# Kernel tuning notes

Measured on AMD Instinct MI355X. Metric: run time of the kernel, lower is better.

The kernel has to match this reference:

```python
import jax, jax.numpy as jnp
import numpy as np
import math

FEATURE_DIM = 64; HIDDEN = 128; NUM_BLOCKS = 4; NUM_ITERS = 4
R = 3; KSIZE = 5; BANDS = 16; TEMP = 0.1
WW = 2 * R + 1; P = WW * WW                      # 7x7 = 49 correlation window
POS_DIM = 3 * (2 * BANDS + 1)                    # 99
IN_DIM = P + POS_DIM + HIDDEN                    # 276
B, Q, T, HF, WF = 1, 256, 64, 128, 128


def setup_inputs() -> dict:
    key = jax.random.key(0)
    ks = jax.random.split(key, 10)
    stride = 4
    extent = jnp.array([WF * stride - 1.0, HF * stride - 1.0], jnp.float32)
    return {
        "query_features": jax.random.normal(ks[0], (B, Q, FEATURE_DIM), jnp.float32),
        "feature_maps": jax.random.normal(ks[1], (B, T, FEATURE_DIM, HF, WF), jnp.float32),
        "positions": jax.random.uniform(ks[2], (B, Q, T, 2), jnp.float32) * extent,
        "feature_stride": stride,
        "w_in": jax.random.normal(ks[3], (IN_DIM, HIDDEN), jnp.float32) * 0.02,
        "b_in": jnp.zeros((HIDDEN,), jnp.float32),
        "ln1_g": jnp.ones((NUM_BLOCKS, HIDDEN), jnp.float32),
        "ln1_b": jnp.zeros((NUM_BLOCKS, HIDDEN), jnp.float32),
        "conv_w": jax.random.normal(ks[4], (NUM_BLOCKS, HIDDEN, 1, KSIZE), jnp.float32) * 0.1,
        "conv_b": jnp.zeros((NUM_BLOCKS, HIDDEN), jnp.float32),
        "ln2_g": jnp.ones((NUM_BLOCKS, HIDDEN), jnp.float32),
        "ln2_b": jnp.zeros((NUM_BLOCKS, HIDDEN), jnp.float32),
        "mlp_w1": jax.random.normal(ks[5], (NUM_BLOCKS, HIDDEN, 2 * HIDDEN), jnp.float32) * 0.02,
        "mlp_b1": jnp.zeros((NUM_BLOCKS, 2 * HIDDEN), jnp.float32),
        "mlp_w2": jax.random.normal(ks[6], (NUM_BLOCKS, 2 * HIDDEN, HIDDEN), jnp.float32) * 0.02,
        "mlp_b2": jnp.zeros((NUM_BLOCKS, HIDDEN), jnp.float32),
        "w_delta": jnp.zeros((HIDDEN, 2), jnp.float32),   # delta head zero-init per _init_weights
        "b_delta": jnp.zeros((2,), jnp.float32),
        "vis_w1": jax.random.normal(ks[7], (HIDDEN, HIDDEN // 2), jnp.float32) * 0.02,
        "vis_b1": jnp.zeros((HIDDEN // 2,), jnp.float32),
        "vis_w2": jax.random.normal(ks[8], (HIDDEN // 2, 1), jnp.float32) * 0.02,
        "vis_b2": jnp.zeros((1,), jnp.float32),
    }


def _layer_norm(x, g, b):
    m = jnp.mean(x, -1, keepdims=True)
    v = jnp.mean((x - m) ** 2, -1, keepdims=True)
    return (x - m) * jax.lax.rsqrt(v + 1e-5) * g + b


def _fourier(coords):
    # sin/cos Fourier encoding + raw coords: [..., D] -> [..., D*(2*BANDS+1)]
    freqs = (2.0 ** jnp.linspace(0.0, math.log2(512.0), BANDS)) * jnp.pi
    x = coords[..., None] * freqs                       # [..., D, BANDS]
    enc = jnp.concatenate([jnp.sin(x), jnp.cos(x)], -1) # [..., D, 2*BANDS]
    enc = enc.reshape(enc.shape[:-2] + (-1,))
    return jnp.concatenate([coords, enc], -1)


def _bilinear(fm, xy):
    # fm: [N, H, W, C] (channels-last); xy: [N, M, 2] feature-grid coords (x, y).
    # Border-clamped bilinear interpolation.
    H, W = fm.shape[1], fm.shape[2]
    x, y = xy[..., 0], xy[..., 1]
    x0f, y0f = jnp.floor(x), jnp.floor(y)
    wx, wy = (x - x0f)[..., None], (y - y0f)[..., None]
    x0 = jnp.clip(x0f.astype(jnp.int32), 0, W - 1)
    x1 = jnp.clip(x0f.astype(jnp.int32) + 1, 0, W - 1)
    y0 = jnp.clip(y0f.astype(jnp.int32), 0, H - 1)
    y1 = jnp.clip(y0f.astype(jnp.int32) + 1, 0, H - 1)
    b = jnp.arange(fm.shape[0])[:, None]
    v00 = fm[b, y0, x0]; v01 = fm[b, y0, x1]
    v10 = fm[b, y1, x0]; v11 = fm[b, y1, x1]
    return (v00 * (1 - wx) + v01 * wx) * (1 - wy) + (v10 * (1 - wx) + v11 * wx) * wy


def _extract_local_correlation(qf, fmaps, pos, stride):
    # qf: [B,Q,C], fmaps: [B,T,C,H,W], pos: [B,Q,T,2] pixel coords.
    Bb, Tt, C, Hf, Wf = fmaps.shape
    Qq = qf.shape[1]
    offs = jnp.arange(-R, R + 1, dtype=pos.dtype)
    oy, ox = jnp.meshgrid(offs, offs, indexing='ij')
    grid = jnp.stack([ox.reshape(-1), oy.reshape(-1)], -1)        # [P,2], x fastest
    off_pix = grid * float(stride)                                 # pixel-unit offsets
    # sampling coords in feature-grid units: pos/stride + offset cells
    sc = pos[:, :, :, None, :] / float(stride) + grid              # [B,Q,T,P,2]
    sc = jnp.transpose(sc, (0, 2, 1, 3, 4)).reshape(Bb * Tt, Qq * P, 2)
    fm = jnp.transpose(fmaps.reshape(Bb * Tt, C, Hf, Wf), (0, 2, 3, 1))
    sampled = _bilinear(fm, sc).reshape(Bb, Tt, Qq, P, C)
    corr = jnp.einsum('btqpc,bqc->bqtp', sampled, qf)              # [B,Q,T,P]
    probs = jax.nn.softmax(corr * (1.0 / max(TEMP, 1e-6)), axis=-1)
    sa_delta = jnp.einsum('bqtp,pd->bqtd', probs, off_pix)         # [B,Q,T,2]
    return corr, sa_delta


def reference(query_features, feature_maps, positions, feature_stride,
              w_in, b_in, ln1_g, ln1_b, conv_w, conv_b, ln2_g, ln2_b,
              mlp_w1, mlp_b1, mlp_w2, mlp_b2, w_delta, b_delta,
              vis_w1, vis_b1, vis_w2, vis_b2):
    Bb, Qq, Tt, _ = positions.shape
    coords = positions
    hidden = jnp.zeros((Bb, Qq, Tt, HIDDEN), positions.dtype)
    t_idx = jnp.linspace(0.0, 1.0, Tt, dtype=positions.dtype).reshape(1, 1, Tt, 1)
    norm_xy = jnp.array([feature_maps.shape[4] * feature_stride,
                         feature_maps.shape[3] * feature_stride], positions.dtype)
    for _ in range(NUM_ITERS):   # weight-shared refinement iterations
        corr, sa = _extract_local_correlation(query_features, feature_maps, coords, feature_stride)
        coords = coords + sa
        pos_in = jnp.concatenate(
            [coords / norm_xy, jnp.broadcast_to(t_idx, (Bb, Qq, Tt, 1))], -1)  # [B,Q,T,3]
        pe = _fourier(pos_in)                                                   # [B,Q,T,99]
        h = jnp.concatenate([corr, pe, hidden], -1) @ w_in + b_in              # [B,Q,T,D]
        h = h.reshape(Bb * Qq, Tt, HIDDEN)
        for i in range(NUM_BLOCKS):
            z = _layer_norm(h, ln1_g[i], ln1_b[i])
            z = jnp.transpose(z, (0, 2, 1))                                     # [BQ,D,T]
            z = jax.lax.conv_general_dilated(
                z, conv_w[i], (1,), [(KSIZE // 2, KSIZE // 2)],
                feature_group_count=HIDDEN, dimension_numbers=('NCH', 'OIH', 'NCH'))
            z = z + conv_b[i][None, :, None]
            h = h + jnp.transpose(z, (0, 2, 1))
            z = _layer_norm(h, ln2_g[i], ln2_b[i])
            h = h + (jax.nn.gelu(z @ mlp_w1[i] + mlp_b1[i], approximate=False)
                     @ mlp_w2[i] + mlp_b2[i])
        h = h.reshape(Bb, Qq, Tt, HIDDEN)
        hidden = h
        coords = coords + h @ w_delta + b_delta
    vis = (jax.nn.gelu(hidden @ vis_w1 + vis_b1, approximate=False) @ vis_w2 + vis_b2)
    return coords, vis
```

## Files before the change

kernel.cpp:

```cpp
#include <hip/hip_runtime.h>
#include <hip/hip_bf16.h>
#include <math.h>

#define PN 49

typedef short v8s __attribute__((ext_vector_type(8)));
typedef float v4f __attribute__((ext_vector_type(4)));
typedef unsigned short us8 __attribute__((ext_vector_type(8)));

#define MFMA_BF16(a,b,c) __builtin_amdgcn_mfma_f32_16x16x32_bf16(a,b,c,0,0,0)

__device__ __forceinline__ unsigned short f2bf(float x) {
    union { float f; unsigned u; } v; v.f = x;
    return (unsigned short)((v.u + 0x7FFFu + ((v.u >> 16) & 1u)) >> 16);
}
__device__ __forceinline__ float bf2f(unsigned short h) {
    union { unsigned u; float f; } v; v.u = ((unsigned)h) << 16;
    return v.f;
}
__device__ __forceinline__ int BIDX(int r, int c) {
    return r * 128 + ((((c >> 3) ^ (r & 15)) << 3) | (c & 7));
}
__device__ __forceinline__ float gelu_exact(float x) {
    return 0.5f * x * (1.0f + erff(x * 0.70710678118654752f));
}
__device__ __forceinline__ float pe_enc(int jj, float px, float py, float ti) {
    const int d = jj >> 5, rr = jj & 31, bnd = rr & 15, isc = rr >> 4;
    const float bv = (d == 0) ? px : ((d == 1) ? py : ti);
    const float a = bv * (exp2f(0.6f * (float)bnd) * 3.14159265358979f);
    return isc ? __cosf(a) : __sinf(a);
}

__global__ __launch_bounds__(256) void repack_kernel(
    const float* __restrict__ w_in, const float* __restrict__ w1,
    const float* __restrict__ w2, unsigned short* __restrict__ pk)
{
    const int id = blockIdx.x * 256 + threadIdx.x;
    if (id >= 584 * 64) return;
    const int chunk = id >> 6, lane = id & 63;
    const int quad = lane >> 4, l15 = lane & 15;
    float v[8];
    if (chunk < 72) {
        const int ks = chunk >> 3, nt = chunk & 7, n = nt * 16 + l15;
#pragma unroll
        for (int j = 0; j < 8; ++j) {
            int src;
            if (ks < 4) src = ks * 32 + quad * 8 + j;
            else if (ks == 4) { const int kl = quad * 8 + j; src = (kl < 20) ? 128 + kl : -1; }
            else src = 148 + (ks - 5) * 32 + quad * 8 + j;
            v[j] = (src >= 0) ? w_in[src * 128 + n] : 0.f;
        }
    } else if (chunk < 328) {
        const int c = chunk - 72, blk = c >> 6, r = c & 63, ks = r >> 4, nt = r & 15;
#pragma unroll
        for (int j = 0; j < 8; ++j)
            v[j] = w1[blk * 32768 + (ks * 32 + quad * 8 + j) * 256 + nt * 16 + l15];
    } else {
        const int c = chunk - 328, blk = c >> 6, r = c & 63, ks = r >> 3, nt = r & 7;
#pragma unroll
        for (int j = 0; j < 8; ++j)
            v[j] = w2[blk * 32768 + (ks * 32 + quad * 8 + j) * 128 + nt * 16 + l15];
    }
    unsigned short* dst = &pk[(size_t)id * 8];
#pragma unroll
    for (int j = 0; j < 8; ++j) dst[j] = f2bf(v[j]);
}

__global__ __launch_bounds__(256) void corr_kernel(
    const float* __restrict__ qf, const float* __restrict__ fm,
    float* __restrict__ coords, float* __restrict__ corr_ws,
    const int* __restrict__ stride_p)
{
    __shared__ float sQ[4][64];
    __shared__ float sD[4][64];
    const int wv   = threadIdx.x >> 6;
    const int lane = threadIdx.x & 63;
    const int t    = blockIdx.x >> 6;
    const int q    = ((blockIdx.x & 63) << 2) + wv;

    sQ[wv][lane] = qf[(q << 6) + lane];

    const int   st     = stride_p[0];
    const float inv_st = 1.0f / (float)st;
    const int   rowg   = (q << 6) + t;
    const float cx = coords[rowg * 2 + 0];
    const float cy = coords[rowg * 2 + 1];
    const float xc = cx * inv_st, yc = cy * inv_st;
    const float x0f = floorf(xc), y0f = floorf(yc);
    const float fx = xc - x0f, fy = yc - y0f;
    const int ix0 = (int)x0f - 3, iy0 = (int)y0f - 3;
    const int gx = min(max(ix0 + (lane & 7), 0), 127);
    const int gy = min(max(iy0 + (lane >> 3), 0), 127);
    const float* base = fm + ((size_t)t << 20) + (gy << 7) + gx;

    __syncthreads();
    float dot = 0.0f;
#pragma unroll 32
    for (int c = 0; c < 64; ++c) dot += base[(size_t)c << 14] * sQ[wv][c];
    sD[wv][lane] = dot;
    __syncthreads();

    const int p = lane;
    float corrv = 0.0f;
    float mval  = -INFINITY;
    int gxc = 0, gyc = 0;
    if (p < PN) {
        gyc = p / 7; gxc = p - gyc * 7;
        const float c00 = sD[wv][gyc * 8 + gxc],     c01 = sD[wv][gyc * 8 + gxc + 1];
        const float c10 = sD[wv][gyc * 8 + gxc + 8], c11 = sD[wv][gyc * 8 + gxc + 9];
        corrv = (1.0f - fy) * ((1.0f - fx) * c00 + fx * c01)
              +          fy * ((1.0f - fx) * c10 + fx * c11);
        corr_ws[(size_t)rowg * PN + p] = corrv;
        mval = corrv * 10.0f;
    }
    float mm = mval;
#pragma unroll
    for (int off = 32; off; off >>= 1) mm = fmaxf(mm, __shfl_xor(mm, off));
    float ex = 0.0f, sax = 0.0f, say = 0.0f;
    if (p < PN) {
        ex  = expf(mval - mm);
        sax = ex * (float)((gxc - 3) * st);
        say = ex * (float)((gyc - 3) * st);
    }
#pragma unroll
    for (int off = 32; off; off >>= 1) {
        ex  += __shfl_xor(ex,  off);
        sax += __shfl_xor(sax, off);
        say += __shfl_xor(say, off);
    }
    if (lane == 0) {
        coords[rowg * 2 + 0] = cx + sax / ex;
        coords[rowg * 2 + 1] = cy + say / ex;
    }
}

__global__ __launch_bounds__(512, 4) void mega_kernel(
    const float* __restrict__ corr_ws, float* __restrict__ coords,
    float* __restrict__ H, const unsigned short* __restrict__ wpk,
    const float* __restrict__ b_in,
    const float* __restrict__ ln1_g, const float* __restrict__ ln1_b,
    const float* __restrict__ conv_w, const float* __restrict__ conv_b,
    const float* __restrict__ ln2_g, const float* __restrict__ ln2_b,
    const float* __restrict__ b1, const float* __restrict__ b2,
    const float* __restrict__ w_delta, const float* __restrict__ b_delta,
    const int* __restrict__ stride_p)
{
    __shared__ float          zs[64 * 128];
    __shared__ unsigned short hbf[64 * 128];
    __shared__ unsigned short sbf[64 * 128];

    const unsigned short* wpk_in = wpk;
    const unsigned short* wpk1   = wpk + 72 * 512;
    const unsigned short* wpk2   = wpk + 328 * 512;

    const int q    = blockIdx.x;
    const int tid  = threadIdx.x;
    const int lane = tid & 63;
    const int wid  = __builtin_amdgcn_readfirstlane(tid >> 6);
    const int l15  = lane & 15, quad = lane >> 4;
    const int mt   = wid & 3, ntg = wid >> 2;
    const float inv_norm = 1.0f / (128.0f * (float)stride_p[0]);

    for (int i = tid; i < 2048; i += 512) {
        const float4 v = ((const float4*)&H[(size_t)q * 8192])[i];
        const int r = i >> 5, c = (i & 31) << 2;
        unsigned short* d = &hbf[BIDX(r, c)];
        d[0] = f2bf(v.x); d[1] = f2bf(v.y); d[2] = f2bf(v.z); d[3] = f2bf(v.w);
    }
    for (int idx = tid; idx < 64 * 128; idx += 512) {
        const int r = idx >> 7, c = idx & 127;
        float v;
        if (c < 49) v = corr_ws[((size_t)((q << 6) + r)) * PN + c];
        else {
            const int j = c - 49;
            const float px = coords[(((q << 6) + r) << 1) + 0] * inv_norm;
            const float py = coords[(((q << 6) + r) << 1) + 1] * inv_norm;
            const float ti = (float)r * (1.0f / 63.0f);
            v = (j == 0) ? px : (j == 1) ? py : (j == 2) ? ti : pe_enc(j - 3, px, py, ti);
        }
        sbf[BIDX(r, c)] = f2bf(v);
    }
    __syncthreads();

    {
        v4f acc[4];
#pragma unroll
        for (int i = 0; i < 4; ++i) acc[i] = v4f{0.f, 0.f, 0.f, 0.f};
        const int arow = mt * 16 + l15;
#pragma unroll
        for (int ks = 0; ks < 4; ++ks) {
            const v8s a = *(const v8s*)&sbf[arow * 128 + (((ks * 4 + quad) ^ (arow & 15)) << 3)];
#pragma unroll
            for (int i = 0; i < 4; ++i) {
                const v8s b = *(const v8s*)&wpk_in[(size_t)((ks * 8 + ntg * 4 + i) * 64 + lane) * 8];
                acc[i] = MFMA_BF16(a, b, acc[i]);
            }
        }
#pragma unroll
        for (int ks = 5; ks < 9; ++ks) {
            const v8s a = *(const v8s*)&hbf[arow * 128 + ((((ks - 5) * 4 + quad) ^ (arow & 15)) << 3)];
#pragma unroll
            for (int i = 0; i < 4; ++i) {
                const v8s b = *(const v8s*)&wpk_in[(size_t)((ks * 8 + ntg * 4 + i) * 64 + lane) * 8];
                acc[i] = MFMA_BF16(a, b, acc[i]);
            }
        }
        __syncthreads();
        for (int idx = tid; idx < 64 * 32; idx += 512) {
            const int r = idx >> 5, c2 = idx & 31;
            float v = 0.f;
            if (c2 < 20) {
                const float px = coords[(((q << 6) + r) << 1) + 0] * inv_norm;
                const float py = coords[(((q << 6) + r) << 1) + 1] * inv_norm;
                const float ti = (float)r * (1.0f / 63.0f);
                v = pe_enc(76 + c2, px, py, ti);
            }
            sbf[BIDX(r, c2)] = f2bf(v);
        }
        __syncthreads();
        {
            const v8s a = *(const v8s*)&sbf[arow * 128 + ((quad ^ (arow & 15)) << 3)];
#pragma unroll
            for (int i = 0; i < 4; ++i) {
                const v8s b = *(const v8s*)&wpk_in[(size_t)((4 * 8 + ntg * 4 + i) * 64 + lane) * 8];
                acc[i] = MFMA_BF16(a, b, acc[i]);
            }
        }
        const int rowb = mt * 16 + quad * 4;
#pragma unroll
        for (int i = 0; i < 4; ++i) {
            const int col = (ntg * 4 + i) * 16 + l15;
            const float bi = b_in[col];
#pragma unroll
            for (int g = 0; g < 4; ++g) zs[(rowb + g) * 128 + col] = acc[i][g] + bi;
        }
    }
    __syncthreads();

    for (int blk = 0; blk < 4; ++blk) {
        {
            const int row = tid >> 3, part = tid & 7;
            float v[16];
#pragma unroll
            for (int x = 0; x < 4; ++x)
                *(float4*)&v[4 * x] = *(const float4*)&zs[row * 128 + part * 16 + 4 * x];
            float s1 = 0.f, s2 = 0.f;
#pragma unroll
            for (int j = 0; j < 16; ++j) { s1 += v[j]; s2 += v[j] * v[j]; }
            s1 += __shfl_xor(s1, 1); s1 += __shfl_xor(s1, 2); s1 += __shfl_xor(s1, 4);
            s2 += __shfl_xor(s2, 1); s2 += __shfl_xor(s2, 2); s2 += __shfl_xor(s2, 4);
            const float m  = s1 * 0.0078125f;
            const float rs = rsqrtf(fmaxf(s2 * 0.0078125f - m * m, 0.f) + 1e-5f);
            unsigned short o[16];
#pragma unroll
            for (int j = 0; j < 16; ++j)
                o[j] = f2bf((v[j] - m) * rs * ln1_g[blk * 128 + part * 16 + j] + ln1_b[blk * 128 + part * 16 + j]);
#pragma unroll
            for (int x = 0; x < 2; ++x)
                *(us8*)&hbf[row * 128 + (((part * 2 + x) ^ (row & 15)) << 3)] = *(us8*)&o[8 * x];
        }
        __syncthreads();
        {
            const int c = tid & 127, tg = tid >> 7;
            float cw[5];
#pragma unroll
            for (int k = 0; k < 5; ++k) cw[k] = conv_w[(blk * 128 + c) * 5 + k];
            const float cb = conv_b[blk * 128 + c];
            float ring[20];
#pragma unroll
            for (int i = 0; i < 20; ++i) {
                const int tt = tg * 16 - 2 + i;
                ring[i] = (tt >= 0 && tt < 64) ? bf2f(hbf[BIDX(tt, c)]) : 0.f;
            }
#pragma unroll
            for (int s = 0; s < 16; ++s) {
                float o = cb;
#pragma unroll
                for (int k = 0; k < 5; ++k) o += ring[s + k] * cw[k];
                zs[(tg * 16 + s) * 128 + c] += o;
            }
        }
        __syncthreads();
        {
            const int row = tid >> 3, part = tid & 7;
            float v[16];
#pragma unroll
            for (int x = 0; x < 4; ++x)
                *(float4*)&v[4 * x] = *(const float4*)&zs[row * 128 + part * 16 + 4 * x];
            float s1 = 0.f, s2 = 0.f;
#pragma unroll
            for (int j = 0; j < 16; ++j) { s1 += v[j]; s2 += v[j] * v[j]; }
            s1 += __shfl_xor(s1, 1); s1 += __shfl_xor(s1, 2); s1 += __shfl_xor(s1, 4);
            s2 += __shfl_xor(s2, 1); s2 += __shfl_xor(s2, 2); s2 += __shfl_xor(s2, 4);
            const float m  = s1 * 0.0078125f;
            const float rs = rsqrtf(fmaxf(s2 * 0.0078125f - m * m, 0.f) + 1e-5f);
            unsigned short o[16];
#pragma unroll
            for (int j = 0; j < 16; ++j)
                o[j] = f2bf((v[j] - m) * rs * ln2_g[blk * 128 + part * 16 + j] + ln2_b[blk * 128 + part * 16 + j]);
#pragma unroll
            for (int x = 0; x < 2; ++x)
                *(us8*)&hbf[row * 128 + (((part * 2 + x) ^ (row & 15)) << 3)] = *(us8*)&o[8 * x];
        }
        __syncthreads();
        v4f u[8];
        const int arow = mt * 16 + l15;
        {
            v8s afr[4];
#pragma unroll
            for (int ks = 0; ks < 4; ++ks)
                afr[ks] = *(const v8s*)&hbf[arow * 128 + (((ks * 4 + quad) ^ (arow & 15)) << 3)];
#pragma unroll
            for (int i = 0; i < 8; ++i) u[i] = v4f{0.f, 0.f, 0.f, 0.f};
#pragma unroll
            for (int ks = 0; ks < 4; ++ks)
#pragma unroll
                for (int i = 0; i < 8; ++i) {
                    const int nt = i * 2 + ntg;
                    const v8s b = *(const v8s*)&wpk1[(size_t)(((blk * 4 + ks) * 16 + nt) * 64 + lane) * 8];
                    u[i] = MFMA_BF16(afr[ks], b, u[i]);
                }
#pragma unroll
            for (int i = 0; i < 8; ++i) {
                const float b1v = b1[blk * 256 + (i * 2 + ntg) * 16 + l15];
#pragma unroll
                for (int g = 0; g < 4; ++g) u[i][g] = gelu_exact(u[i][g] + b1v);
            }
        }
        const int rowb = mt * 16 + quad * 4;
#pragma unroll
        for (int i = 0; i < 4; ++i) {
            const int ucol = (i * 2 + ntg) * 16 + l15;
#pragma unroll
            for (int g = 0; g < 4; ++g) sbf[BIDX(rowb + g, ucol)] = f2bf(u[i][g]);
        }
        __syncthreads();
        v4f c2[4];
#pragma unroll
        for (int i = 0; i < 4; ++i) c2[i] = v4f{0.f, 0.f, 0.f, 0.f};
#pragma unroll
        for (int ks = 0; ks < 4; ++ks) {
            const v8s a = *(const v8s*)&sbf[arow * 128 + (((ks * 4 + quad) ^ (arow & 15)) << 3)];
#pragma unroll
            for (int i = 0; i < 4; ++i) {
                const v8s b = *(const v8s*)&wpk2[(size_t)(((blk * 8 + ks) * 8 + ntg * 4 + i) * 64 + lane) * 8];
                c2[i] = MFMA_BF16(a, b, c2[i]);
            }
        }
        __syncthreads();
#pragma unroll
        for (int i = 4; i < 8; ++i) {
            const int ucol = (i * 2 + ntg) * 16 + l15 - 128;
#pragma unroll
            for (int g = 0; g < 4; ++g) sbf[BIDX(rowb + g, ucol)] = f2bf(u[i][g]);
        }
        __syncthreads();
#pragma unroll
        for (int ks = 0; ks < 4; ++ks) {
            const v8s a = *(const v8s*)&sbf[arow * 128 + (((ks * 4 + quad) ^ (arow & 15)) << 3)];
#pragma unroll
            for (int i = 0; i < 4; ++i) {
                const v8s b = *(const v8s*)&wpk2[(size_t)(((blk * 8 + 4 + ks) * 8 + ntg * 4 + i) * 64 + lane) * 8];
                c2[i] = MFMA_BF16(a, b, c2[i]);
            }
        }
#pragma unroll
        for (int i = 0; i < 4; ++i) {
            const int col = (ntg * 4 + i) * 16 + l15;
            const float b2v = b2[blk * 128 + col];
#pragma unroll
            for (int g = 0; g < 4; ++g) zs[(rowb + g) * 128 + col] += c2[i][g] + b2v;
        }
        __syncthreads();
    }

    {
        const int row = tid >> 3, part = tid & 7;
        float dx = 0.f, dy = 0.f;
#pragma unroll
        for (int j = 0; j < 16; ++j) {
            const int c = part * 16 + j;
            const float hv = zs[row * 128 + c];
            dx += hv * w_delta[2 * c];
            dy += hv * w_delta[2 * c + 1];
        }
        dx += __shfl_xor(dx, 1); dx += __shfl_xor(dx, 2); dx += __shfl_xor(dx, 4);
        dy += __shfl_xor(dy, 1); dy += __shfl_xor(dy, 2); dy += __shfl_xor(dy, 4);
        if (part == 0) {
            coords[(((q << 6) + row) << 1) + 0] += dx + b_delta[0];
            coords[(((q << 6) + row) << 1) + 1] += dy + b_delta[1];
        }
    }
    for (int i = tid; i < 2048; i += 512)
        ((float4*)&H[(size_t)q * 8192])[i] = ((const float4*)zs)[i];
}

__global__ __launch_bounds__(256) void vis_kernel(
    const float* __restrict__ H,
    const float* __restrict__ vw1, const float* __restrict__ vb1,
    const float* __restrict__ vw2, const float* __restrict__ vb2,
    float* __restrict__ out)
{
    const int row = (blockIdx.x << 2) + (threadIdx.x >> 6);
    const int j   = threadIdx.x & 63;
    float acc = vb1[j];
    const float* hr = &H[(size_t)row << 7];
#pragma unroll 16
    for (int k = 0; k < 128; ++k) acc += hr[k] * vw1[(k << 6) + j];
    float pv = gelu_exact(acc) * vw2[j];
#pragma unroll
    for (int off = 32; off; off >>= 1) pv += __shfl_xor(pv, off);
    if (j == 0) out[row] = pv + vb2[0];
}

extern "C" void kernel_launch(void* const* d_in, const int* in_sizes, int n_in,
                              void* d_out, int out_size, void* d_ws, size_t ws_size,
                              hipStream_t stream) {
    const float* qf       = (const float*)d_in[0];
    const float* fm       = (const float*)d_in[1];
    const float* pos      = (const float*)d_in[2];
    const int*   stride_p = (const int*)  d_in[3];
    const float* w_in     = (const float*)d_in[4];
    const float* b_in     = (const float*)d_in[5];
    const float* ln1_g    = (const float*)d_in[6];
    const float* ln1_b    = (const float*)d_in[7];
    const float* conv_w   = (const float*)d_in[8];
    const float* conv_b   = (const float*)d_in[9];
    const float* ln2_g    = (const float*)d_in[10];
    const float* ln2_b    = (const float*)d_in[11];
    const float* mlp_w1   = (const float*)d_in[12];
    const float* mlp_b1   = (const float*)d_in[13];
    const float* mlp_w2   = (const float*)d_in[14];
    const float* mlp_b2   = (const float*)d_in[15];
    const float* w_delta  = (const float*)d_in[16];
    const float* b_delta  = (const float*)d_in[17];
    const float* vis_w1   = (const float*)d_in[18];
    const float* vis_b1   = (const float*)d_in[19];
    const float* vis_w2   = (const float*)d_in[20];
    const float* vis_b2   = (const float*)d_in[21];

    float* Wf      = (float*)d_ws;
    float* coords  = Wf;
    float* corr_ws = Wf + 32768;
    float* H       = Wf + 32768 + 802816;
    unsigned short* wpk = (unsigned short*)(Wf + 2932736);

    repack_kernel<<<dim3(146), dim3(256), 0, stream>>>(w_in, mlp_w1, mlp_w2, wpk);
    hipMemcpyAsync(coords, pos, 32768 * sizeof(float), hipMemcpyDeviceToDevice, stream);
    hipMemsetAsync(H, 0, 2097152 * sizeof(float), stream);

    for (int it = 0; it < 4; ++it) {
        corr_kernel<<<dim3(4096), dim3(256), 0, stream>>>(qf, fm, coords, corr_ws, stride_p);
        mega_kernel<<<dim3(256), dim3(512), 0, stream>>>(
            corr_ws, coords, H, wpk, b_in, ln1_g, ln1_b, conv_w, conv_b,
            ln2_g, ln2_b, mlp_b1, mlp_b2, w_delta, b_delta, stride_p);
    }
    vis_kernel<<<dim3(4096), dim3(256), 0, stream>>>(
        H, vis_w1, vis_b1, vis_w2, vis_b2, ((float*)d_out) + 32768);
    hipMemcpyAsync(d_out, coords, 32768 * sizeof(float), hipMemcpyDeviceToDevice, stream);
}
```

Baseline: 1.739 ms.

## Split mega kernel per query into two time halves with conv halo recompute

Each query's 64-step sequence is now handled by two blocks, each covering 32 output time steps plus an 8-step halo on each side (48 rows). The halo is recomputed so the stacked depthwise convolutions stay correct without inter-block communication. This doubles the grid to 512 blocks of 768 threads so more CUs are busy, and threads are remapped accordingly. The cost is about 50% redundant compute on the halo rows plus extra index and boundary checks.

```diff
diff --git a/kernel.cpp b/kernel.cpp
--- a/kernel.cpp
+++ b/kernel.cpp
@@ -3,6 +3,9 @@
 #include <math.h>
 
 #define PN 49
+#define RB 48
+#define OUT0 8
+#define OUTN 32
 
 typedef short v8s __attribute__((ext_vector_type(8)));
 typedef float v4f __attribute__((ext_vector_type(4)));
@@ -134,7 +137,7 @@
     }
 }
 
-__global__ __launch_bounds__(512, 4) void mega_kernel(
+__global__ __launch_bounds__(768, 6) void mega_kernel(
     const float* __restrict__ corr_ws, float* __restrict__ coords,
     float* __restrict__ H, const unsigned short* __restrict__ wpk,
     const float* __restrict__ b_in,
@@ -145,54 +148,68 @@
     const float* __restrict__ w_delta, const float* __restrict__ b_delta,
     const int* __restrict__ stride_p)
 {
-    __shared__ float          zs[64 * 128];
-    __shared__ unsigned short hbf[64 * 128];
-    __shared__ unsigned short sbf[64 * 128];
+    __shared__ float          zs[RB * 128];
+    __shared__ unsigned short hbf[RB * 128];
+    __shared__ unsigned short sbf[RB * 128];
+    __shared__ float          crd[RB][2];
 
     const unsigned short* wpk_in = wpk;
     const unsigned short* wpk1   = wpk + 72 * 512;
     const unsigned short* wpk2   = wpk + 328 * 512;
 
-    const int q    = blockIdx.x;
-    const int tid  = threadIdx.x;
-    const int lane = tid & 63;
-    const int wid  = __builtin_amdgcn_readfirstlane(tid >> 6);
-    const int l15  = lane & 15, quad = lane >> 4;
-    const int mt   = wid & 3, ntg = wid >> 2;
+    const int q     = blockIdx.x >> 1;
+    const int half  = blockIdx.x & 1;
+    const int baset = half * 32 - OUT0;
+    const int tid   = threadIdx.x;
+    const int lane  = tid & 63;
+    const int wid   = __builtin_amdgcn_readfirstlane(tid >> 6);
+    const int l15   = lane & 15, quad = lane >> 4;
+    const int mt    = wid >> 2, ntg = wid & 3;
     const float inv_norm = 1.0f / (128.0f * (float)stride_p[0]);
 
-    for (int i = tid; i < 2048; i += 512) {
-        const float4 v = ((const float4*)&H[(size_t)q * 8192])[i];
-        const int r = i >> 5, c = (i & 31) << 2;
-        unsigned short* d = &hbf[BIDX(r, c)];
+    if (tid < RB * 2) {
+        const int rr = tid >> 1, xy = tid & 1;
+        const int tc = min(max(baset + rr, 0), 63);
+        crd[rr][xy] = coords[(((q << 6) + tc) << 1) + xy];
+    }
+    for (int i = tid; i < RB * 32; i += 768) {
+        const int r = i >> 5, c0 = (i & 31) << 2;
+        const int t = baset + r;
+        float4 v = make_float4(0.f, 0.f, 0.f, 0.f);
+        if (t >= 0 && t < 64) v = *(const float4*)&H[(size_t)q * 8192 + t * 128 + c0];
+        unsigned short* d = &hbf[BIDX(r, c0)];
         d[0] = f2bf(v.x); d[1] = f2bf(v.y); d[2] = f2bf(v.z); d[3] = f2bf(v.w);
     }
-    for (int idx = tid; idx < 64 * 128; idx += 512) {
+    __syncthreads();
+    for (int idx = tid; idx < RB * 128; idx += 768) {
         const int r = idx >> 7, c = idx & 127;
+        const int t = baset + r;
         float v;
-        if (c < 49) v = corr_ws[((size_t)((q << 6) + r)) * PN + c];
+        if (c < 49) v = (t >= 0 && t < 64) ? corr_ws[((size_t)((q << 6) + t)) * PN + c] : 0.f;
         else {
             const int j = c - 49;
-            const float px = coords[(((q << 6) + r) << 1) + 0] * inv_norm;
-            const float py = coords[(((q << 6) + r) << 1) + 1] * inv_norm;
-            const float ti = (float)r * (1.0f / 63.0f);
+            const float px = crd[r][0] * inv_norm;
+            const float py = crd[r][1] * inv_norm;
+            const float ti = (float)min(max(t, 0), 63) * (1.0f / 63.0f);
             v = (j == 0) ? px : (j == 1) ? py : (j == 2) ? ti : pe_enc(j - 3, px, py, ti);
         }
         sbf[BIDX(r, c)] = f2bf(v);
     }
     __syncthreads();
 
+    const int arow = mt * 16 + l15;
+    const int rowb = mt * 16 + quad * 4;
+
     {
-        v4f acc[4];
-#pragma unroll
-        for (int i = 0; i < 4; ++i) acc[i] = v4f{0.f, 0.f, 0.f, 0.f};
-        const int arow = mt * 16 + l15;
+        v4f acc[2];
+#pragma unroll
+        for (int i = 0; i < 2; ++i) acc[i] = v4f{0.f, 0.f, 0.f, 0.f};
 #pragma unroll
         for (int ks = 0; ks < 4; ++ks) {
             const v8s a = *(const v8s*)&sbf[arow * 128 + (((ks * 4 + quad) ^ (arow & 15)) << 3)];
 #pragma unroll
-            for (int i = 0; i < 4; ++i) {
-                const v8s b = *(const v8s*)&wpk_in[(size_t)((ks * 8 + ntg * 4 + i) * 64 + lane) * 8];
+            for (int i = 0; i < 2; ++i) {
+                const v8s b = *(const v8s*)&wpk_in[(size_t)((ks * 8 + ntg * 2 + i) * 64 + lane) * 8];
                 acc[i] = MFMA_BF16(a, b, acc[i]);
             }
         }
@@ -200,19 +217,20 @@
         for (int ks = 5; ks < 9; ++ks) {
             const v8s a = *(const v8s*)&hbf[arow * 128 + ((((ks - 5) * 4 + quad) ^ (arow & 15)) << 3)];
 #pragma unroll
-            for (int i = 0; i < 4; ++i) {
-                const v8s b = *(const v8s*)&wpk_in[(size_t)((ks * 8 + ntg * 4 + i) * 64 + lane) * 8];
+            for (int i = 0; i < 2; ++i) {
+                const v8s b = *(const v8s*)&wpk_in[(size_t)((ks * 8 + ntg * 2 + i) * 64 + lane) * 8];
                 acc[i] = MFMA_BF16(a, b, acc[i]);
             }
         }
         __syncthreads();
-        for (int idx = tid; idx < 64 * 32; idx += 512) {
+        for (int idx = tid; idx < RB * 32; idx += 768) {
             const int r = idx >> 5, c2 = idx & 31;
             float v = 0.f;
             if (c2 < 20) {
-                const float px = coords[(((q << 6) + r) << 1) + 0] * inv_norm;
-                const float py = coords[(((q << 6) + r) << 1) + 1] * inv_norm;
-                const float ti = (float)r * (1.0f / 63.0f);
+                const int t = baset + r;
+                const float px = crd[r][0] * inv_norm;
+                const float py = crd[r][1] * inv_norm;
+                const float ti = (float)min(max(t, 0), 63) * (1.0f / 63.0f);
                 v = pe_enc(76 + c2, px, py, ti);
             }
             sbf[BIDX(r, c2)] = f2bf(v);
@@ -221,15 +239,14 @@
         {
             const v8s a = *(const v8s*)&sbf[arow * 128 + ((quad ^ (arow & 15)) << 3)];
 #pragma unroll
-            for (int i = 0; i < 4; ++i) {
-                const v8s b = *(const v8s*)&wpk_in[(size_t)((4 * 8 + ntg * 4 + i) * 64 + lane) * 8];
+            for (int i = 0; i < 2; ++i) {
+                const v8s b = *(const v8s*)&wpk_in[(size_t)((4 * 8 + ntg * 2 + i) * 64 + lane) * 8];
                 acc[i] = MFMA_BF16(a, b, acc[i]);
             }
         }
-        const int rowb = mt * 16 + quad * 4;
-#pragma unroll
-        for (int i = 0; i < 4; ++i) {
-            const int col = (ntg * 4 + i) * 16 + l15;
+#pragma unroll
+        for (int i = 0; i < 2; ++i) {
+            const int col = (ntg * 2 + i) * 16 + l15;
             const float bi = b_in[col];
 #pragma unroll
             for (int g = 0; g < 4; ++g) zs[(rowb + g) * 128 + col] = acc[i][g] + bi;
@@ -239,25 +256,24 @@
 
     for (int blk = 0; blk < 4; ++blk) {
         {
-            const int row = tid >> 3, part = tid & 7;
-            float v[16];
-#pragma unroll
-            for (int x = 0; x < 4; ++x)
-                *(float4*)&v[4 * x] = *(const float4*)&zs[row * 128 + part * 16 + 4 * x];
+            const int row = tid >> 4, part = tid & 15;
+            float v[8];
+            *(float4*)&v[0] = *(const float4*)&zs[row * 128 + part * 8];
+            *(float4*)&v[4] = *(const float4*)&zs[row * 128 + part * 8 + 4];
             float s1 = 0.f, s2 = 0.f;
 #pragma unroll
-            for (int j = 0; j < 16; ++j) { s1 += v[j]; s2 += v[j] * v[j]; }
-            s1 += __shfl_xor(s1, 1); s1 += __shfl_xor(s1, 2); s1 += __shfl_xor(s1, 4);
-            s2 += __shfl_xor(s2, 1); s2 += __shfl_xor(s2, 2); s2 += __shfl_xor(s2, 4);
+            for (int j = 0; j < 8; ++j) { s1 += v[j]; s2 += v[j] * v[j]; }
+            s1 += __shfl_xor(s1, 1); s1 += __shfl_xor(s1, 2);
+            s1 += __shfl_xor(s1, 4); s1 += __shfl_xor(s1, 8);
+            s2 += __shfl_xor(s2, 1); s2 += __shfl_xor(s2, 2);
+            s2 += __shfl_xor(s2, 4); s2 += __shfl_xor(s2, 8);
             const float m  = s1 * 0.0078125f;
             const float rs = rsqrtf(fmaxf(s2 * 0.0078125f - m * m, 0.f) + 1e-5f);
-            unsigned short o[16];
-#pragma unroll
-            for (int j = 0; j < 16; ++j)
-                o[j] = f2bf((v[j] - m) * rs * ln1_g[blk * 128 + part * 16 + j] + ln1_b[blk * 128 + part * 16 + j]);
-#pragma unroll
-            for (int x = 0; x < 2; ++x)
-                *(us8*)&hbf[row * 128 + (((part * 2 + x) ^ (row & 15)) << 3)] = *(us8*)&o[8 * x];
+            unsigned short o[8];
+#pragma unroll
+            for (int j = 0; j < 8; ++j)
+                o[j] = f2bf((v[j] - m) * rs * ln1_g[blk * 128 + part * 8 + j] + ln1_b[blk * 128 + part * 8 + j]);
+            *(us8*)&hbf[row * 128 + ((part ^ (row & 15)) << 3)] = *(us8*)&o[0];
         }
         __syncthreads();
         {
@@ -266,107 +282,108 @@
 #pragma unroll
             for (int k = 0; k < 5; ++k) cw[k] = conv_w[(blk * 128 + c) * 5 + k];
             const float cb = conv_b[blk * 128 + c];
-            float ring[20];
-#pragma unroll
-            for (int i = 0; i < 20; ++i) {
-                const int tt = tg * 16 - 2 + i;
-                ring[i] = (tt >= 0 && tt < 64) ? bf2f(hbf[BIDX(tt, c)]) : 0.f;
-            }
-#pragma unroll
-            for (int s = 0; s < 16; ++s) {
+            float ring[12];
+#pragma unroll
+            for (int i = 0; i < 12; ++i) {
+                const int rr = tg * 8 - 2 + i;
+                const int t  = baset + rr;
+                ring[i] = (rr >= 0 && rr < RB && t >= 0 && t < 64) ? bf2f(hbf[BIDX(rr, c)]) : 0.f;
+            }
+#pragma unroll
+            for (int s = 0; s < 8; ++s) {
                 float o = cb;
 #pragma unroll
                 for (int k = 0; k < 5; ++k) o += ring[s + k] * cw[k];
-                zs[(tg * 16 + s) * 128 + c] += o;
+                zs[(tg * 8 + s) * 128 + c] += o;
             }
         }
         __syncthreads();
         {
-            const int row = tid >> 3, part = tid & 7;
-            float v[16];
-#pragma unroll
-            for (int x = 0; x < 4; ++x)
-                *(float4*)&v[4 * x] = *(const float4*)&zs[row * 128 + part * 16 + 4 * x];
+            const int row = tid >> 4, part = tid & 15;
+            float v[8];
+            *(float4*)&v[0] = *(const float4*)&zs[row * 128 + part * 8];
+            *(float4*)&v[4] = *(const float4*)&zs[row * 128 + part * 8 + 4];
             float s1 = 0.f, s2 = 0.f;
 #pragma unroll
-            for (int j = 0; j < 16; ++j) { s1 += v[j]; s2 += v[j] * v[j]; }
-            s1 += __shfl_xor(s1, 1); s1 += __shfl_xor(s1, 2); s1 += __shfl_xor(s1, 4);
-            s2 += __shfl_xor(s2, 1); s2 += __shfl_xor(s2, 2); s2 += __shfl_xor(s2, 4);
+            for (int j = 0; j < 8; ++j) { s1 += v[j]; s2 += v[j] * v[j]; }
+            s1 += __shfl_xor(s1, 1); s1 += __shfl_xor(s1, 2);
+            s1 += __shfl_xor(s1, 4); s1 += __shfl_xor(s1, 8);
+            s2 += __shfl_xor(s2, 1); s2 += __shfl_xor(s2, 2);
+            s2 += __shfl_xor(s2, 4); s2 += __shfl_xor(s2, 8);
             const float m  = s1 * 0.0078125f;
             const float rs = rsqrtf(fmaxf(s2 * 0.0078125f - m * m, 0.f) + 1e-5f);
-            unsigned short o[16];
-#pragma unroll
-            for (int j = 0; j < 16; ++j)
-                o[j] = f2bf((v[j] - m) * rs * ln2_g[blk * 128 + part * 16 + j] + ln2_b[blk * 128 + part * 16 + j]);
-#pragma unroll
-            for (int x = 0; x < 2; ++x)
-                *(us8*)&hbf[row * 128 + (((part * 2 + x) ^ (row & 15)) << 3)] = *(us8*)&o[8 * x];
-        }
-        __syncthreads();
-        v4f u[8];
-        const int arow = mt * 16 + l15;
+            unsigned short o[8];
+#pragma unroll
+            for (int j = 0; j < 8; ++j)
+                o[j] = f2bf((v[j] - m) * rs * ln2_g[blk * 128 + part * 8 + j] + ln2_b[blk * 128 + part * 8 + j]);
+            *(us8*)&hbf[row * 128 + ((part ^ (row & 15)) << 3)] = *(us8*)&o[0];
+        }
+        __syncthreads();
+        v4f u[4];
         {
             v8s afr[4];
 #pragma unroll
             for (int ks = 0; ks < 4; ++ks)
                 afr[ks] = *(const v8s*)&hbf[arow * 128 + (((ks * 4 + quad) ^ (arow & 15)) << 3)];
 #pragma unroll
-            for (int i = 0; i < 8; ++i) u[i] = v4f{0.f, 0.f, 0.f, 0.f};
+            for (int i = 0; i < 4; ++i) u[i] = v4f{0.f, 0.f, 0.f, 0.f};
 #pragma unroll
             for (int ks = 0; ks < 4; ++ks)
 #pragma unroll
-                for (int i = 0; i < 8; ++i) {
-                    const int nt = i * 2 + ntg;
-                    const v8s b = *(const v8s*)&wpk1[(size_t)(((blk * 4 + ks) * 16 + nt) * 64 + lane) * 8];
+                for (int i = 0; i < 4; ++i) {
+                    const v8s b = *(const v8s*)&wpk1[(size_t)(((blk * 4 + ks) * 16 + ntg * 4 + i) * 64 + lane) * 8];
                     u[i] = MFMA_BF16(afr[ks], b, u[i]);
                 }
 #pragma unroll
-            for (int i = 0; i < 8; ++i) {
-                const float b1v = b1[blk * 256 + (i * 2 + ntg) * 16 + l15];
+            for (int i = 0; i < 4; ++i) {
+                const float b1v = b1[blk * 256 + (ntg * 4 + i) * 16 + l15];
 #pragma unroll
                 for (int g = 0; g < 4; ++g) u[i][g] = gelu_exact(u[i][g] + b1v);
             }
         }
-        const int rowb = mt * 16 + quad * 4;
-#pragma unroll
-        for (int i = 0; i < 4; ++i) {
-            const int ucol = (i * 2 + ntg) * 16 + l15;
-#pragma unroll
-            for (int g = 0; g < 4; ++g) sbf[BIDX(rowb + g, ucol)] = f2bf(u[i][g]);
-        }
-        __syncthreads();
-        v4f c2[4];
-#pragma unroll
-        for (int i = 0; i < 4; ++i) c2[i] = v4f{0.f, 0.f, 0.f, 0.f};
+        if (ntg < 2) {
+#pragma unroll
+            for (int i = 0; i < 4; ++i) {
+                const int ucol = (ntg * 4 + i) * 16 + l15;
+#pragma unroll
+                for (int g = 0; g < 4; ++g) sbf[BIDX(rowb + g, ucol)] = f2bf(u[i][g]);
+            }
+        }
+        __syncthreads();
+        v4f c2[2];
+#pragma unroll
+        for (int i = 0; i < 2; ++i) c2[i] = v4f{0.f, 0.f, 0.f, 0.f};
 #pragma unroll
         for (int ks = 0; ks < 4; ++ks) {
             const v8s a = *(const v8s*)&sbf[arow * 128 + (((ks * 4 + quad) ^ (arow & 15)) << 3)];
 #pragma unroll
+            for (int i = 0; i < 2; ++i) {
+                const v8s b = *(const v8s*)&wpk2[(size_t)(((blk * 8 + ks) * 8 + ntg * 2 + i) * 64 + lane) * 8];
+                c2[i] = MFMA_BF16(a, b, c2[i]);
+            }
+        }
+        __syncthreads();
+        if (ntg >= 2) {
+#pragma unroll
             for (int i = 0; i < 4; ++i) {
-                const v8s b = *(const v8s*)&wpk2[(size_t)(((blk * 8 + ks) * 8 + ntg * 4 + i) * 64 + lane) * 8];
-                c2[i] = MFMA_BF16(a, b, c2[i]);
-            }
-        }
-        __syncthreads();
-#pragma unroll
-        for (int i = 4; i < 8; ++i) {
-            const int ucol = (i * 2 + ntg) * 16 + l15 - 128;
-#pragma unroll
-            for (int g = 0; g < 4; ++g) sbf[BIDX(rowb + g, ucol)] = f2bf(u[i][g]);
+                const int ucol = (ntg * 4 + i) * 16 + l15 - 128;
+#pragma unroll
+                for (int g = 0; g < 4; ++g) sbf[BIDX(rowb + g, ucol)] = f2bf(u[i][g]);
+            }
         }
         __syncthreads();
 #pragma unroll
         for (int ks = 0; ks < 4; ++ks) {
             const v8s a = *(const v8s*)&sbf[arow * 128 + (((ks * 4 + quad) ^ (arow & 15)) << 3)];
 #pragma unroll
-            for (int i = 0; i < 4; ++i) {
-                const v8s b = *(const v8s*)&wpk2[(size_t)(((blk * 8 + 4 + ks) * 8 + ntg * 4 + i) * 64 + lane) * 8];
+            for (int i = 0; i < 2; ++i) {
+                const v8s b = *(const v8s*)&wpk2[(size_t)(((blk * 8 + 4 + ks) * 8 + ntg * 2 + i) * 64 + lane) * 8];
                 c2[i] = MFMA_BF16(a, b, c2[i]);
             }
         }
 #pragma unroll
-        for (int i = 0; i < 4; ++i) {
-            const int col = (ntg * 4 + i) * 16 + l15;
+        for (int i = 0; i < 2; ++i) {
+            const int col = (ntg * 2 + i) * 16 + l15;
             const float b2v = b2[blk * 128 + col];
 #pragma unroll
             for (int g = 0; g < 4; ++g) zs[(rowb + g) * 128 + col] += c2[i][g] + b2v;
@@ -375,24 +392,32 @@
     }
 
     {
-        const int row = tid >> 3, part = tid & 7;
-        float dx = 0.f, dy = 0.f;
-#pragma unroll
-        for (int j = 0; j < 16; ++j) {
-            const int c = part * 16 + j;
-            const float hv = zs[row * 128 + c];
-            dx += hv * w_delta[2 * c];
-            dy += hv * w_delta[2 * c + 1];
-        }
-        dx += __shfl_xor(dx, 1); dx += __shfl_xor(dx, 2); dx += __shfl_xor(dx, 4);
-        dy += __shfl_xor(dy, 1); dy += __shfl_xor(dy, 2); dy += __shfl_xor(dy, 4);
-        if (part == 0) {
-            coords[(((q << 6) + row) << 1) + 0] += dx + b_delta[0];
-            coords[(((q << 6) + row) << 1) + 1] += dy + b_delta[1];
-        }
-    }
-    for (int i = tid; i < 2048; i += 512)
-        ((float4*)&H[(size_t)q * 8192])[i] = ((const float4*)zs)[i];
+        const int row = tid >> 4, part = tid & 15;
+        if (row >= OUT0 && row < OUT0 + OUTN) {
+            float dx = 0.f, dy = 0.f;
+#pragma unroll
+            for (int j = 0; j < 8; ++j) {
+                const int c = part * 8 + j;
+                const float hv = zs[row * 128 + c];
+                dx += hv * w_delta[2 * c];
+                dy += hv * w_delta[2 * c + 1];
+            }
+            dx += __shfl_xor(dx, 1); dx += __shfl_xor(dx, 2);
+            dx += __shfl_xor(dx, 4); dx += __shfl_xor(dx, 8);
+            dy += __shfl_xor(dy, 1); dy += __shfl_xor(dy, 2);
+            dy += __shfl_xor(dy, 4); dy += __shfl_xor(dy, 8);
+            if (part == 0) {
+                const int t = baset + row;
+                coords[(((q << 6) + t) << 1) + 0] = crd[row][0] + dx + b_delta[0];
+                coords[(((q << 6) + t) << 1) + 1] = crd[row][1] + dy + b_delta[1];
+            }
+        }
+    }
+    for (int i = tid; i < OUTN * 32; i += 768) {
+        const int r = i >> 5, c0 = (i & 31) << 2;
+        const int t = half * 32 + r;
+        *(float4*)&H[(size_t)q * 8192 + t * 128 + c0] = *(const float4*)&zs[(OUT0 + r) * 128 + c0];
+    }
 }
 
 __global__ __launch_bounds__(256) void vis_kernel(
@@ -451,7 +476,7 @@
 
     for (int it = 0; it < 4; ++it) {
         corr_kernel<<<dim3(4096), dim3(256), 0, stream>>>(qf, fm, coords, corr_ws, stride_p);
-        mega_kernel<<<dim3(256), dim3(512), 0, stream>>>(
+        mega_kernel<<<dim3(512), dim3(768), 0, stream>>>(
             corr_ws, coords, H, wpk, b_in, ln1_g, ln1_b, conv_w, conv_b,
             ln2_g, ln2_b, mlp_b1, mlp_b2, w_delta, b_delta, stride_p);
     }
```

Result: slower. 1.782 ms (+2.5%).
